# Kernel tuning notes

Hardware: AMD Instinct MI355X
Metric: run time of the kernel (lower is better)

The kernel has to match this reference:

```python
import jax, jax.numpy as jnp
import numpy as np

DEPTH, LENGTH, WIDTH, NUM_CLASSES = 8, 32, 32, 8
STD_POSITION = 1.0
STD_INTENSITY = 3.0


def setup_inputs() -> dict:
    key = jax.random.key(0)
    k1, k2 = jax.random.split(key)
    patch = jax.random.normal(k1, (DEPTH, LENGTH, WIDTH), dtype=jnp.float32)
    prob = jax.random.uniform(k2, (DEPTH, LENGTH, WIDTH, NUM_CLASSES), dtype=jnp.float32)
    return {"patch": patch, "prob": prob, "k": NUM_CLASSES}


def _dist_weight():
    # Matches torch.meshgrid(arange(depth), arange(length), arange(width)) with 'ij' indexing,
    # then row-major flatten. dist_weight[i,j] = exp(-||pos_i - pos_j||^2 / std_position^2)
    gx, gy, gz = jnp.meshgrid(
        jnp.arange(DEPTH, dtype=jnp.float32),
        jnp.arange(LENGTH, dtype=jnp.float32),
        jnp.arange(WIDTH, dtype=jnp.float32),
        indexing="ij",
    )
    x, y, z = gx.ravel(), gy.ravel(), gz.ravel()  # each [n]
    sq = (
        jnp.square(x[:, None] - x[None, :])
        + jnp.square(y[:, None] - y[None, :])
        + jnp.square(z[:, None] - z[None, :])
    )  # [n, n]
    return jnp.exp(-sq / (STD_POSITION ** 2))


def reference(patch, prob, k):
    n = DEPTH * LENGTH * WIDTH
    f = patch.reshape(-1)  # [n]
    # intensity_weight is .detach()ed in the original -> stop_gradient for faithfulness
    intensity = jax.lax.stop_gradient(
        jnp.exp(-jnp.square((f[:, None] - f[None, :]) / STD_INTENSITY))
    )  # [n, n]
    W = intensity * _dist_weight()  # [n, n]

    P = prob.reshape(n, k)  # row-major flatten matches torch.reshape of prob[:,:,:,t]
    WP = W @ P  # [n, k]
    num = jnp.sum(P * WP, axis=0)            # per-class p^T W p
    den = P.T @ (W @ jnp.ones((n,), W.dtype))  # per-class p^T W 1
    loss = jnp.float32(k) - jnp.sum(num / den)
    return loss.astype(jnp.float32)
```

## Files before the change

kernel.cpp:

```cpp
#include <hip/hip_runtime.h>

#define N       8192
#define NCLS    8
#define ROWS_PB 4
#define GRID    (N / ROWS_PB)

__global__ __launch_bounds__(256) void sncut_rows(const float* __restrict__ f,
                                                  const float* __restrict__ P,
                                                  float* __restrict__ partials)
{
    const int tid  = threadIdx.x;
    const int lane = tid & 63;
    const int wave = tid >> 6;
    const int i    = blockIdx.x * ROWS_PB + wave;

    const int zi = i & 31, yi = (i >> 5) & 31, xi = i >> 10;
    const float fi = f[i];

    float v0 = 0.f, v1 = 0.f, v2 = 0.f, v3 = 0.f;
    float v4 = 0.f, v5 = 0.f, v6 = 0.f, v7 = 0.f;
    float vr = 0.f;

    if (lane < 63) {
        const int oy = lane / 9, oz = lane - oy * 9;

        int y0 = yi - 3; y0 = y0 < 0 ? 0 : (y0 > 25 ? 25 : y0);
        int z0 = zi - 4; z0 = z0 < 0 ? 0 : (z0 > 23 ? 23 : z0);
        int x0 = xi - 3; x0 = x0 < 0 ? 0 : (x0 > 1 ? 1 : x0);

        const int yj = y0 + oy, zj = z0 + oz;
        const int dy = yi - yj, dz = zi - zj;
        const float base = (float)(dy * dy + dz * dz);
        const int jcol = (yj << 5) + zj;

        #pragma unroll
        for (int k = 0; k < 7; ++k) {
            const int xj = x0 + k;
            const int dx = xi - xj;
            const int j  = (xj << 10) + jcol;
            const float df  = fi - f[j];
            const float arg = df * df * (1.0f / 9.0f) + (base + (float)(dx * dx));
            const float w   = __expf(-arg);
            const float4 p0 = *reinterpret_cast<const float4*>(P + (size_t)j * NCLS);
            const float4 p1 = *reinterpret_cast<const float4*>(P + (size_t)j * NCLS + 4);
            v0 += w * p0.x; v1 += w * p0.y; v2 += w * p0.z; v3 += w * p0.w;
            v4 += w * p1.x; v5 += w * p1.y; v6 += w * p1.z; v7 += w * p1.w;
            vr += w;
        }
    }

    float vals[9] = {v0, v1, v2, v3, v4, v5, v6, v7, vr};
    #pragma unroll
    for (int v = 0; v < 9; ++v) {
        float x = vals[v];
        #pragma unroll
        for (int off = 32; off > 0; off >>= 1)
            x += __shfl_down(x, off, 64);
        vals[v] = x;
    }

    __shared__ float sh[ROWS_PB][16];
    if (lane == 0) {
        const float4 p0 = *reinterpret_cast<const float4*>(P + (size_t)i * NCLS);
        const float4 p1 = *reinterpret_cast<const float4*>(P + (size_t)i * NCLS + 4);
        sh[wave][0]  = p0.x * vals[0];
        sh[wave][1]  = p0.y * vals[1];
        sh[wave][2]  = p0.z * vals[2];
        sh[wave][3]  = p0.w * vals[3];
        sh[wave][4]  = p1.x * vals[4];
        sh[wave][5]  = p1.y * vals[5];
        sh[wave][6]  = p1.z * vals[6];
        sh[wave][7]  = p1.w * vals[7];
        sh[wave][8]  = p0.x * vals[8];
        sh[wave][9]  = p0.y * vals[8];
        sh[wave][10] = p0.z * vals[8];
        sh[wave][11] = p0.w * vals[8];
        sh[wave][12] = p1.x * vals[8];
        sh[wave][13] = p1.y * vals[8];
        sh[wave][14] = p1.z * vals[8];
        sh[wave][15] = p1.w * vals[8];
    }
    __syncthreads();
    if (tid < 16) {
        const float s = sh[0][tid] + sh[1][tid] + sh[2][tid] + sh[3][tid];
        partials[(size_t)blockIdx.x * 16 + tid] = s;
    }
}

__global__ __launch_bounds__(1024) void sncut_final(const float* __restrict__ partials,
                                                    float* __restrict__ out)
{
    const int tid = threadIdx.x;
    const int e = tid & 15;
    const int g = tid >> 4;

    float s = 0.f;
    #pragma unroll
    for (int m = 0; m < GRID / 64; ++m)
        s += partials[(size_t)(g + m * 64) * 16 + e];

    __shared__ float acc[64][17];
    acc[g][e] = s;
    __syncthreads();

    __shared__ float sums[16];
    if (tid < 16) {
        float t = 0.f;
        #pragma unroll
        for (int g2 = 0; g2 < 64; ++g2) t += acc[g2][tid];
        sums[tid] = t;
    }
    __syncthreads();
    if (tid == 0) {
        float loss = (float)NCLS;
        #pragma unroll
        for (int t = 0; t < NCLS; ++t) loss -= sums[t] / sums[NCLS + t];
        out[0] = loss;
    }
}

extern "C" void kernel_launch(void* const* d_in, const int* in_sizes, int n_in,
                              void* d_out, int out_size, void* d_ws, size_t ws_size,
                              hipStream_t stream) {
    const float* f = (const float*)d_in[0];
    const float* P = (const float*)d_in[1];

    float* partials = (float*)d_ws;

    sncut_rows<<<GRID, 256, 0, stream>>>(f, P, partials);
    sncut_final<<<1, 1024, 0, stream>>>(partials, (float*)d_out);
}
```

Before: 68.05 us.

## Process four rows per wave and amortize cross-lane reductions

Each wave now loops over four consecutive rows, multiplying by the row's own probabilities per lane and accumulating 16 per-class numerator/denominator sums before a single wave shuffle reduction. This cuts the shuffle reduction cost per row and shrinks the grid and partials buffer by four, with the final reduction kernel resized accordingly. The trade-off is fewer waves in flight, which may reduce latency hiding for the gather loads, plus more live registers.

```diff
diff --git a/kernel.cpp b/kernel.cpp
--- a/kernel.cpp
+++ b/kernel.cpp
@@ -1,9 +1,11 @@
 #include <hip/hip_runtime.h>
 
-#define N       8192
-#define NCLS    8
-#define ROWS_PB 4
-#define GRID    (N / ROWS_PB)
+#define N        8192
+#define NCLS     8
+#define RPW      4
+#define WPB      4
+#define ROWS_PB  (RPW * WPB)
+#define GRID     (N / ROWS_PB)
 
 __global__ __launch_bounds__(256) void sncut_rows(const float* __restrict__ f,
                                                   const float* __restrict__ P,
@@ -12,46 +14,60 @@
     const int tid  = threadIdx.x;
     const int lane = tid & 63;
     const int wave = tid >> 6;
-    const int i    = blockIdx.x * ROWS_PB + wave;
 
-    const int zi = i & 31, yi = (i >> 5) & 31, xi = i >> 10;
-    const float fi = f[i];
+    const int oy = lane / 9, oz = lane - oy * 9;
+    const bool active = (lane < 63);
 
-    float v0 = 0.f, v1 = 0.f, v2 = 0.f, v3 = 0.f;
-    float v4 = 0.f, v5 = 0.f, v6 = 0.f, v7 = 0.f;
-    float vr = 0.f;
+    float u0=0.f,u1=0.f,u2=0.f,u3=0.f,u4=0.f,u5=0.f,u6=0.f,u7=0.f;
+    float d0=0.f,d1=0.f,d2=0.f,d3=0.f,d4=0.f,d5=0.f,d6=0.f,d7=0.f;
 
-    if (lane < 63) {
-        const int oy = lane / 9, oz = lane - oy * 9;
+    const int ibase = blockIdx.x * ROWS_PB + wave * RPW;
 
-        int y0 = yi - 3; y0 = y0 < 0 ? 0 : (y0 > 25 ? 25 : y0);
-        int z0 = zi - 4; z0 = z0 < 0 ? 0 : (z0 > 23 ? 23 : z0);
-        int x0 = xi - 3; x0 = x0 < 0 ? 0 : (x0 > 1 ? 1 : x0);
+    for (int r = 0; r < RPW; ++r) {
+        const int i  = ibase + r;
+        const int zi = i & 31, yi = (i >> 5) & 31, xi = i >> 10;
+        const float fi = f[i];
 
-        const int yj = y0 + oy, zj = z0 + oz;
-        const int dy = yi - yj, dz = zi - zj;
-        const float base = (float)(dy * dy + dz * dz);
-        const int jcol = (yj << 5) + zj;
+        float wp0=0.f,wp1=0.f,wp2=0.f,wp3=0.f,wp4=0.f,wp5=0.f,wp6=0.f,wp7=0.f;
+        float rs = 0.f;
 
-        #pragma unroll
-        for (int k = 0; k < 7; ++k) {
-            const int xj = x0 + k;
-            const int dx = xi - xj;
-            const int j  = (xj << 10) + jcol;
-            const float df  = fi - f[j];
-            const float arg = df * df * (1.0f / 9.0f) + (base + (float)(dx * dx));
-            const float w   = __expf(-arg);
-            const float4 p0 = *reinterpret_cast<const float4*>(P + (size_t)j * NCLS);
-            const float4 p1 = *reinterpret_cast<const float4*>(P + (size_t)j * NCLS + 4);
-            v0 += w * p0.x; v1 += w * p0.y; v2 += w * p0.z; v3 += w * p0.w;
-            v4 += w * p1.x; v5 += w * p1.y; v6 += w * p1.z; v7 += w * p1.w;
-            vr += w;
+        if (active) {
+            int y0 = yi - 3; y0 = y0 < 0 ? 0 : (y0 > 25 ? 25 : y0);
+            int z0 = zi - 4; z0 = z0 < 0 ? 0 : (z0 > 23 ? 23 : z0);
+            int x0 = xi - 3; x0 = x0 < 0 ? 0 : (x0 > 1 ? 1 : x0);
+
+            const int yj = y0 + oy, zj = z0 + oz;
+            const int dy = yi - yj, dz = zi - zj;
+            const float base = (float)(dy * dy + dz * dz);
+            const int jcol = (yj << 5) + zj;
+
+            #pragma unroll
+            for (int k = 0; k < 7; ++k) {
+                const int xj = x0 + k;
+                const int dx = xi - xj;
+                const int j  = (xj << 10) + jcol;
+                const float df  = fi - f[j];
+                const float arg = df * df * (1.0f / 9.0f) + (base + (float)(dx * dx));
+                const float w   = __expf(-arg);
+                const float4 p0 = *reinterpret_cast<const float4*>(P + (size_t)j * NCLS);
+                const float4 p1 = *reinterpret_cast<const float4*>(P + (size_t)j * NCLS + 4);
+                wp0 += w * p0.x; wp1 += w * p0.y; wp2 += w * p0.z; wp3 += w * p0.w;
+                wp4 += w * p1.x; wp5 += w * p1.y; wp6 += w * p1.z; wp7 += w * p1.w;
+                rs  += w;
+            }
         }
+
+        const float4 pi0 = *reinterpret_cast<const float4*>(P + (size_t)i * NCLS);
+        const float4 pi1 = *reinterpret_cast<const float4*>(P + (size_t)i * NCLS + 4);
+        u0 += pi0.x * wp0; u1 += pi0.y * wp1; u2 += pi0.z * wp2; u3 += pi0.w * wp3;
+        u4 += pi1.x * wp4; u5 += pi1.y * wp5; u6 += pi1.z * wp6; u7 += pi1.w * wp7;
+        d0 += pi0.x * rs;  d1 += pi0.y * rs;  d2 += pi0.z * rs;  d3 += pi0.w * rs;
+        d4 += pi1.x * rs;  d5 += pi1.y * rs;  d6 += pi1.z * rs;  d7 += pi1.w * rs;
     }
 
-    float vals[9] = {v0, v1, v2, v3, v4, v5, v6, v7, vr};
+    float vals[16] = {u0,u1,u2,u3,u4,u5,u6,u7,d0,d1,d2,d3,d4,d5,d6,d7};
     #pragma unroll
-    for (int v = 0; v < 9; ++v) {
+    for (int v = 0; v < 16; ++v) {
         float x = vals[v];
         #pragma unroll
         for (int off = 32; off > 0; off >>= 1)
@@ -59,36 +75,19 @@
         vals[v] = x;
     }
 
-    __shared__ float sh[ROWS_PB][16];
+    __shared__ float sh[WPB][16];
     if (lane == 0) {
-        const float4 p0 = *reinterpret_cast<const float4*>(P + (size_t)i * NCLS);
-        const float4 p1 = *reinterpret_cast<const float4*>(P + (size_t)i * NCLS + 4);
-        sh[wave][0]  = p0.x * vals[0];
-        sh[wave][1]  = p0.y * vals[1];
-        sh[wave][2]  = p0.z * vals[2];
-        sh[wave][3]  = p0.w * vals[3];
-        sh[wave][4]  = p1.x * vals[4];
-        sh[wave][5]  = p1.y * vals[5];
-        sh[wave][6]  = p1.z * vals[6];
-        sh[wave][7]  = p1.w * vals[7];
-        sh[wave][8]  = p0.x * vals[8];
-        sh[wave][9]  = p0.y * vals[8];
-        sh[wave][10] = p0.z * vals[8];
-        sh[wave][11] = p0.w * vals[8];
-        sh[wave][12] = p1.x * vals[8];
-        sh[wave][13] = p1.y * vals[8];
-        sh[wave][14] = p1.z * vals[8];
-        sh[wave][15] = p1.w * vals[8];
+        #pragma unroll
+        for (int v = 0; v < 16; ++v) sh[wave][v] = vals[v];
     }
     __syncthreads();
-    if (tid < 16) {
-        const float s = sh[0][tid] + sh[1][tid] + sh[2][tid] + sh[3][tid];
-        partials[(size_t)blockIdx.x * 16 + tid] = s;
-    }
+    if (tid < 16)
+        partials[(size_t)blockIdx.x * 16 + tid] =
+            sh[0][tid] + sh[1][tid] + sh[2][tid] + sh[3][tid];
 }
 
-__global__ __launch_bounds__(1024) void sncut_final(const float* __restrict__ partials,
-                                                    float* __restrict__ out)
+__global__ __launch_bounds__(512) void sncut_final(const float* __restrict__ partials,
+                                                   float* __restrict__ out)
 {
     const int tid = threadIdx.x;
     const int e = tid & 15;
@@ -96,10 +95,10 @@
 
     float s = 0.f;
     #pragma unroll
-    for (int m = 0; m < GRID / 64; ++m)
-        s += partials[(size_t)(g + m * 64) * 16 + e];
+    for (int m = 0; m < GRID / 32; ++m)
+        s += partials[(size_t)(g + m * 32) * 16 + e];
 
-    __shared__ float acc[64][17];
+    __shared__ float acc[32][17];
     acc[g][e] = s;
     __syncthreads();
 
@@ -107,7 +106,7 @@
     if (tid < 16) {
         float t = 0.f;
         #pragma unroll
-        for (int g2 = 0; g2 < 64; ++g2) t += acc[g2][tid];
+        for (int g2 = 0; g2 < 32; ++g2) t += acc[g2][tid];
         sums[tid] = t;
     }
     __syncthreads();
@@ -128,5 +127,5 @@
     float* partials = (float*)d_ws;
 
     sncut_rows<<<GRID, 256, 0, stream>>>(f, P, partials);
-    sncut_final<<<1, 1024, 0, stream>>>(partials, (float*)d_out);
+    sncut_final<<<1, 512, 0, stream>>>(partials, (float*)d_out);
 }
```

Measured after the change: 68.60 us (median of 2 runs). No clear change (+0.8%).
